# Optimization experiments

Hardware: AMD Instinct MI355X
Metric: run time of the kernel (lower is better)

Reference implementation:

```python
import jax, jax.numpy as jnp
import numpy as np

VOCAB, EMBED, HIDDEN, N_CLASSES = 50257, 128, 256, 2
B = S = 512  # must be equal: the original module only runs when x.size(0)==x.size(1)


def gru_layer(x_seq, Wih, Whh, bih, bhh):
    """PyTorch-equation GRU over time axis 0. x_seq: (T, N, E) -> (T, N, H)."""
    T, N, _ = x_seq.shape
    H = Whh.shape[1]
    xi = x_seq @ Wih.T + bih  # precompute input projections for all steps: (T, N, 3H)

    def step(h, xi_t):
        gh = h @ Whh.T + bhh
        xr, xz, xn = jnp.split(xi_t, 3, axis=-1)
        hr, hz, hn = jnp.split(gh, 3, axis=-1)
        r = jax.nn.sigmoid(xr + hr)
        z = jax.nn.sigmoid(xz + hz)
        n = jnp.tanh(xn + r * hn)
        h_new = (1.0 - z) * n + z * h
        return h_new, h_new

    h0 = jnp.zeros((N, H), dtype=x_seq.dtype)
    _, ys = jax.lax.scan(step, h0, xi)
    return ys


def setup_inputs() -> dict:
    key = jax.random.key(0)
    ks = jax.random.split(key, 12)
    sc = 0.05
    return {
        "x": jax.random.randint(ks[0], (B, S), 0, VOCAB),
        "embed_table": jax.random.normal(ks[1], (VOCAB, EMBED), jnp.float32) * sc,
        "Wih0": jax.random.normal(ks[2], (3 * HIDDEN, EMBED), jnp.float32) * sc,
        "Whh0": jax.random.normal(ks[3], (3 * HIDDEN, HIDDEN), jnp.float32) * sc,
        "bih0": jax.random.normal(ks[4], (3 * HIDDEN,), jnp.float32) * sc,
        "bhh0": jax.random.normal(ks[5], (3 * HIDDEN,), jnp.float32) * sc,
        "Wih1": jax.random.normal(ks[6], (3 * HIDDEN, HIDDEN), jnp.float32) * sc,
        "Whh1": jax.random.normal(ks[7], (3 * HIDDEN, HIDDEN), jnp.float32) * sc,
        "bih1": jax.random.normal(ks[8], (3 * HIDDEN,), jnp.float32) * sc,
        "bhh1": jax.random.normal(ks[9], (3 * HIDDEN,), jnp.float32) * sc,
        "W_out": jax.random.normal(ks[10], (N_CLASSES, HIDDEN), jnp.float32) * sc,
        "b_out": jax.random.normal(ks[11], (N_CLASSES,), jnp.float32) * sc,
    }


def reference(x, embed_table, Wih0, Whh0, bih0, bhh0, Wih1, Whh1, bih1, bhh1, W_out, b_out):
    emb = embed_table[x]                 # (B, S, E)
    # nn.GRU default batch_first=False: dim 0 (=B) is TIME, dim 1 (=S) is batch.
    y = gru_layer(emb, Wih0, Whh0, bih0, bhh0)   # (B, S, H)
    y = gru_layer(y, Wih1, Whh1, bih1, bhh1)     # (B, S, H)
    h_t = y[:, -1, :]                    # (B, H)
    # self.dropout(h_t) in the original discards its result -> no-op.
    logit = h_t @ W_out.T + b_out        # (B, n_classes)
    return logit
```

## Files before the change

kernel.cpp:

```cpp
#include <hip/hip_runtime.h>
#include <hip/hip_fp16.h>

typedef _Float16 f16x2 __attribute__((ext_vector_type(2)));
typedef _Float16 half8 __attribute__((ext_vector_type(8)));

#define TS  512
#define HID 256
#define G3  768
#define EMB 128
#define NB1 8
#define RPB 96
#define CTL 767
#define BSZ 8
#define WAITN 8

__device__ __forceinline__ float sigmoidf_(float x){ return 1.0f/(1.0f+__expf(-x)); }
__device__ __forceinline__ float tanhf_(float x){
  float e = __expf(-2.0f*fabsf(x));
  float t = (1.0f-e)/(1.0f+e);
  return copysignf(t,x);
}

#define SHUF(V,A,B) __builtin_shufflevector(V,V,A,B)
#define WR32(X) X(0,0) X(0,1) X(0,2) X(0,3) X(1,0) X(1,1) X(1,2) X(1,3) \
                X(2,0) X(2,1) X(2,2) X(2,3) X(3,0) X(3,1) X(3,2) X(3,3) \
                X(4,0) X(4,1) X(4,2) X(4,3) X(5,0) X(5,1) X(5,2) X(5,3) \
                X(6,0) X(6,1) X(6,2) X(6,3) X(7,0) X(7,1) X(7,2) X(7,3)

template<int MODE>
__device__ __forceinline__ void rec_layer(const float* __restrict__ Whh,
    const float* __restrict__ bhh, const float* __restrict__ xi,
    _Float16* __restrict__ h16out, float* __restrict__ f32out,
    unsigned* __restrict__ flagB, unsigned* __restrict__ cntWait,
    _Float16 (*hbuf)[8*40], float* gh, float* bhhL)
{
  int tid = threadIdx.x;
  int g   = tid >> 3;
  int o   = tid & 7;

#define WDECL(I,C) half8 w##I##_##C;
  WR32(WDECL)
#define WLOAD(I,C) { \
    const float4* p_ = (const float4*)(Whh + (long)(8*g+(I))*HID + 32*o + 8*(C)); \
    float4 u_ = p_[0], v_ = p_[1]; \
    w##I##_##C = (half8){(_Float16)u_.x,(_Float16)u_.y,(_Float16)u_.z,(_Float16)u_.w, \
                         (_Float16)v_.x,(_Float16)v_.y,(_Float16)v_.z,(_Float16)v_.w}; }
  WR32(WLOAD)

  float hprev = 0.f;
  float xr=0.f, xz=0.f, xn=0.f;
  bhhL[tid] = bhh[tid];
  if (tid < 80) ((half8*)hbuf)[tid] = (half8)(_Float16)0;

  if (tid == CTL){
    while (__hip_atomic_load(&cntWait[0], __ATOMIC_RELAXED, __HIP_MEMORY_SCOPE_AGENT) < WAITN)
      __builtin_amdgcn_s_sleep(1);
    __threadfence();
  }
  __syncthreads();
  if (tid < HID){
    xr = xi[tid]; xz = xi[HID+tid]; xn = xi[2*HID+tid];
  }

  for (int t = 0; t < TS; t++){
    if (tid == CTL && ((t+1) & (BSZ-1)) == 0 && t+1 < TS){
      unsigned b = (unsigned)(t+1) >> 3;
      while (__hip_atomic_load(&cntWait[b], __ATOMIC_RELAXED, __HIP_MEMORY_SCOPE_AGENT) < WAITN)
        __builtin_amdgcn_s_sleep(1);
      __threadfence();
    }

    const half8* hp = (const half8*)(&hbuf[t & 1][o*40]);
    float a0=0.f,a1=0.f,a2=0.f,a3=0.f,a4=0.f,a5=0.f,a6=0.f,a7=0.f;
#define DOT1(I,C,HV) \
    a##I = __builtin_amdgcn_fdot2(SHUF(w##I##_##C,0,1), SHUF(HV,0,1), a##I, false); \
    a##I = __builtin_amdgcn_fdot2(SHUF(w##I##_##C,2,3), SHUF(HV,2,3), a##I, false); \
    a##I = __builtin_amdgcn_fdot2(SHUF(w##I##_##C,4,5), SHUF(HV,4,5), a##I, false); \
    a##I = __builtin_amdgcn_fdot2(SHUF(w##I##_##C,6,7), SHUF(HV,6,7), a##I, false);
#define DOTCHUNK(C) { half8 hv = hp[C]; \
    DOT1(0,C,hv) DOT1(1,C,hv) DOT1(2,C,hv) DOT1(3,C,hv) \
    DOT1(4,C,hv) DOT1(5,C,hv) DOT1(6,C,hv) DOT1(7,C,hv) }
    DOTCHUNK(0) DOTCHUNK(1) DOTCHUNK(2) DOTCHUNK(3)

    bool b0 = o & 1, b1 = o & 2, b2 = o & 4;
    float s, r_;
    s = b0 ? a0 : a1; r_ = __shfl_xor(s, 1, 64); float c0 = (b0 ? a1 : a0) + r_;
    s = b0 ? a2 : a3; r_ = __shfl_xor(s, 1, 64); float c1 = (b0 ? a3 : a2) + r_;
    s = b0 ? a4 : a5; r_ = __shfl_xor(s, 1, 64); float c2 = (b0 ? a5 : a4) + r_;
    s = b0 ? a6 : a7; r_ = __shfl_xor(s, 1, 64); float c3 = (b0 ? a7 : a6) + r_;
    s = b1 ? c0 : c1; r_ = __shfl_xor(s, 2, 64); float d0 = (b1 ? c1 : c0) + r_;
    s = b1 ? c2 : c3; r_ = __shfl_xor(s, 2, 64); float d1 = (b1 ? c3 : c2) + r_;
    s = b2 ? d0 : d1; r_ = __shfl_xor(s, 4, 64); float e  = (b2 ? d1 : d0) + r_;
    gh[tid] = e;
    __syncthreads();

    if (tid < HID){
      float r = sigmoidf_(xr + bhhL[tid] + gh[tid]);
      float z = sigmoidf_(xz + bhhL[HID+tid] + gh[HID+tid]);
      float n = tanhf_(xn + r*(gh[2*HID+tid] + bhhL[2*HID+tid]));
      float hnew = (1.0f - z)*n + z*hprev;
      hprev = hnew;
      if (MODE == 1) f32out[(long)t*HID + tid] = hnew;
      float partner = __shfl_xor(hnew, 1, 64);
      if ((tid & 1) == 0){
        f16x2 p; p.x = (_Float16)hnew; p.y = (_Float16)partner;
        *(f16x2*)(&hbuf[(t+1)&1][(tid>>5)*40 + (tid&31)]) = p;
        if (MODE == 0) *(f16x2*)(h16out + (long)t*HID + tid) = p;
      }
      if (t+1 < TS){
        const float* xp = xi + (long)(t+1)*G3;
        xr = xp[tid]; xz = xp[HID+tid]; xn = xp[2*HID+tid];
      }
    }
    __syncthreads();
    if (MODE == 0 && tid == CTL && ((t+1) & (BSZ-1)) == 0){
      __threadfence();
      __hip_atomic_store(&flagB[t >> 3], 1u, __ATOMIC_RELEASE, __HIP_MEMORY_SCOPE_AGENT);
    }
  }
}

__device__ __forceinline__ void xi1_stage(const float* __restrict__ Wih1,
    const float* __restrict__ bih1, const _Float16* __restrict__ h16,
    float* __restrict__ xi1, unsigned* __restrict__ flagB,
    unsigned* __restrict__ cntB, int slice)
{
  int tid = threadIdx.x;
  int r = tid >> 3, o = tid & 7;
  int row = slice*RPB + r;
  half8 w0,w1,w2,w3;
  {
    const float4* wp = (const float4*)(Wih1 + (long)row*HID + o*32);
    float4 p0=wp[0],p1=wp[1],p2=wp[2],p3=wp[3],p4=wp[4],p5=wp[5],p6=wp[6],p7=wp[7];
    w0 = (half8){(_Float16)p0.x,(_Float16)p0.y,(_Float16)p0.z,(_Float16)p0.w,
                 (_Float16)p1.x,(_Float16)p1.y,(_Float16)p1.z,(_Float16)p1.w};
    w1 = (half8){(_Float16)p2.x,(_Float16)p2.y,(_Float16)p2.z,(_Float16)p2.w,
                 (_Float16)p3.x,(_Float16)p3.y,(_Float16)p3.z,(_Float16)p3.w};
    w2 = (half8){(_Float16)p4.x,(_Float16)p4.y,(_Float16)p4.z,(_Float16)p4.w,
                 (_Float16)p5.x,(_Float16)p5.y,(_Float16)p5.z,(_Float16)p5.w};
    w3 = (half8){(_Float16)p6.x,(_Float16)p6.y,(_Float16)p6.z,(_Float16)p6.w,
                 (_Float16)p7.x,(_Float16)p7.y,(_Float16)p7.z,(_Float16)p7.w};
  }
  float bias = bih1[row];

  for (int b = 0; b < TS/BSZ; b++){
    if (tid == 0){
      while (__hip_atomic_load(&flagB[b], __ATOMIC_RELAXED, __HIP_MEMORY_SCOPE_AGENT) == 0u)
        __builtin_amdgcn_s_sleep(1);
      __threadfence();
    }
    __syncthreads();
    #pragma unroll 4
    for (int u = 0; u < BSZ; u++){
      int t = b*BSZ + u;
      const half8* hp = (const half8*)(h16 + (long)t*HID + o*32);
      half8 h0 = hp[0], h1 = hp[1], h2 = hp[2], h3 = hp[3];
      float acc = 0.f;
#define XDOT(W,H) \
      acc = __builtin_amdgcn_fdot2(SHUF(W,0,1), SHUF(H,0,1), acc, false); \
      acc = __builtin_amdgcn_fdot2(SHUF(W,2,3), SHUF(H,2,3), acc, false); \
      acc = __builtin_amdgcn_fdot2(SHUF(W,4,5), SHUF(H,4,5), acc, false); \
      acc = __builtin_amdgcn_fdot2(SHUF(W,6,7), SHUF(H,6,7), acc, false);
      XDOT(w0,h0) XDOT(w1,h1) XDOT(w2,h2) XDOT(w3,h3)
      acc += __shfl_xor(acc, 1, 64);
      acc += __shfl_xor(acc, 2, 64);
      acc += __shfl_xor(acc, 4, 64);
      if (o == 0) xi1[(long)t*G3 + row] = acc + bias;
    }
    __syncthreads();
    if (tid == 0){
      __threadfence();
      atomicAdd(&cntB[b], 1u);
    }
  }
}

__device__ __forceinline__ void xi0_stage(const int* __restrict__ x,
    const float* __restrict__ emb_tab, const float* __restrict__ Wih0,
    const float* __restrict__ bih0, float* __restrict__ xi0,
    unsigned* __restrict__ cntX, int slice, float* embp)
{
  int tid = threadIdx.x;
  int j = tid >> 3, kk = tid & 7;
  int row = slice*96 + j;
  float w16[16];
  {
    const float4* wp = (const float4*)(Wih0 + (long)row*EMB + kk*16);
    float4 a = wp[0], b = wp[1], c = wp[2], d = wp[3];
    w16[0]=a.x;  w16[1]=a.y;  w16[2]=a.z;  w16[3]=a.w;
    w16[4]=b.x;  w16[5]=b.y;  w16[6]=b.z;  w16[7]=b.w;
    w16[8]=c.x;  w16[9]=c.y;  w16[10]=c.z; w16[11]=c.w;
    w16[12]=d.x; w16[13]=d.y; w16[14]=d.z; w16[15]=d.w;
  }
  float bias = bih0[row];

  for (int t = 0; t < TS; t++){
    if (tid < EMB){
      int idx = x[(long)t*512 + 511];
      embp[tid + (tid >> 4)] = emb_tab[(long)idx*EMB + tid];
    }
    __syncthreads();
    float a = 0.f;
    #pragma unroll
    for (int m = 0; m < 16; m++) a += w16[m] * embp[kk*17 + m];
    a += __shfl_xor(a, 1, 64);
    a += __shfl_xor(a, 2, 64);
    a += __shfl_xor(a, 4, 64);
    if (kk == 0) xi0[(long)t*G3 + row] = a + bias;
    __syncthreads();
    if (((t+1) & (BSZ-1)) == 0 && tid == 0){
      __threadfence();
      atomicAdd(&cntX[t >> 3], 1u);
    }
  }
}

__global__ __launch_bounds__(768, 3)
void pipe_kernel(
    const float* __restrict__ Whh0, const float* __restrict__ bhh0,
    const float* __restrict__ Wih1, const float* __restrict__ bih1,
    const float* __restrict__ Whh1, const float* __restrict__ bhh1,
    const int* __restrict__ x, const float* __restrict__ emb_tab,
    const float* __restrict__ Wih0, const float* __restrict__ bih0,
    float* __restrict__ xi0, _Float16* __restrict__ h1f16,
    float* __restrict__ xi1, float* __restrict__ h2,
    unsigned* __restrict__ flagB, unsigned* __restrict__ cntB,
    unsigned* __restrict__ cntX)
{
  __shared__ __align__(16) _Float16 hbuf[2][8*40];
  __shared__ float gh[G3];
  __shared__ float bhhL[G3];
  __shared__ float embp[136];
  int bid = blockIdx.x;
  if (bid == 0)
    rec_layer<0>(Whh0, bhh0, xi0, h1f16, nullptr, flagB, cntX, hbuf, gh, bhhL);
  else if (bid == 9)
    rec_layer<1>(Whh1, bhh1, xi1, nullptr, h2, flagB, cntB, hbuf, gh, bhhL);
  else if (bid < 9)
    xi1_stage(Wih1, bih1, h1f16, xi1, flagB, cntB, bid - 1);
  else
    xi0_stage(x, emb_tab, Wih0, bih0, xi0, cntX, bid - 10, embp);
}

__global__ __launch_bounds__(1024) void logits_kernel(const float* __restrict__ h2,
    const float* __restrict__ Wout, const float* __restrict__ bout,
    float* __restrict__ out)
{
  __shared__ __align__(16) float wsm[2*HID];
  __shared__ float bs[2];
  int tid = threadIdx.x;
  if (tid < 2*HID) wsm[tid] = Wout[tid];
  if (tid < 2)     bs[tid]  = bout[tid];
  __syncthreads();
  int t = tid >> 1, c = tid & 1;
  const float4* hr = (const float4*)(h2 + (long)t*HID);
  const float4* wr = (const float4*)(wsm + c*HID);
  float acc = bs[c];
  #pragma unroll 8
  for (int m=0;m<HID/4;m++){
    float4 h = hr[m]; float4 wv = wr[m];
    acc += h.x*wv.x + h.y*wv.y + h.z*wv.z + h.w*wv.w;
  }
  out[tid] = acc;
}

extern "C" void kernel_launch(void* const* d_in, const int* in_sizes, int n_in,
                              void* d_out, int out_size, void* d_ws, size_t ws_size,
                              hipStream_t stream)
{
  const int*   x    = (const int*)  d_in[0];
  const float* emb  = (const float*)d_in[1];
  const float* Wih0 = (const float*)d_in[2];
  const float* Whh0 = (const float*)d_in[3];
  const float* bih0 = (const float*)d_in[4];
  const float* bhh0 = (const float*)d_in[5];
  const float* Wih1 = (const float*)d_in[6];
  const float* Whh1 = (const float*)d_in[7];
  const float* bih1 = (const float*)d_in[8];
  const float* bhh1 = (const float*)d_in[9];
  const float* Wout = (const float*)d_in[10];
  const float* bout = (const float*)d_in[11];
  float* out = (float*)d_out;

  char* ws = (char*)d_ws;
  float*     xi0   = (float*)(ws);
  float*     xi1   = (float*)(ws + 1572864);
  _Float16*  h1f16 = (_Float16*)(ws + 3145728);
  float*     h2    = (float*)(ws + 3407872);
  unsigned*  flagB = (unsigned*)(ws + 3932160);
  unsigned*  cntB  = (unsigned*)(ws + 3933184);
  unsigned*  cntX  = (unsigned*)(ws + 3934208);

  hipMemsetAsync(ws + 3932160, 0, 4096, stream);
  pipe_kernel<<<18, 768, 0, stream>>>(Whh0, bhh0, Wih1, bih1, Whh1, bhh1,
                                      x, emb, Wih0, bih0,
                                      xi0, h1f16, xi1, h2, flagB, cntB, cntX);
  logits_kernel<<<1, 1024, 0, stream>>>(h2, Wout, bout, out);
}
```

Measured before the change: 834.9 us.

## Halve pipeline sync block size and fuse logits into layer-2 recurrent block

```diff
diff --git a/kernel.cpp b/kernel.cpp
--- a/kernel.cpp
+++ b/kernel.cpp
@@ -8,10 +8,9 @@
 #define HID 256
 #define G3  768
 #define EMB 128
-#define NB1 8
 #define RPB 96
 #define CTL 767
-#define BSZ 8
+#define BSZ 4
 #define WAITN 8
 
 __device__ __forceinline__ float sigmoidf_(float x){ return 1.0f/(1.0f+__expf(-x)); }
@@ -32,7 +31,9 @@
     const float* __restrict__ bhh, const float* __restrict__ xi,
     _Float16* __restrict__ h16out, float* __restrict__ f32out,
     unsigned* __restrict__ flagB, unsigned* __restrict__ cntWait,
-    _Float16 (*hbuf)[8*40], float* gh, float* bhhL)
+    _Float16 (*hbuf)[8*40], float* gh, float* bhhL,
+    const float* __restrict__ Wout, const float* __restrict__ bout,
+    float* __restrict__ out)
 {
   int tid = threadIdx.x;
   int g   = tid >> 3;
@@ -64,7 +65,7 @@
 
   for (int t = 0; t < TS; t++){
     if (tid == CTL && ((t+1) & (BSZ-1)) == 0 && t+1 < TS){
-      unsigned b = (unsigned)(t+1) >> 3;
+      unsigned b = (unsigned)(t+1) / BSZ;
       while (__hip_atomic_load(&cntWait[b], __ATOMIC_RELAXED, __HIP_MEMORY_SCOPE_AGENT) < WAITN)
         __builtin_amdgcn_s_sleep(1);
       __threadfence();
@@ -115,7 +116,23 @@
     __syncthreads();
     if (MODE == 0 && tid == CTL && ((t+1) & (BSZ-1)) == 0){
       __threadfence();
-      __hip_atomic_store(&flagB[t >> 3], 1u, __ATOMIC_RELEASE, __HIP_MEMORY_SCOPE_AGENT);
+      __hip_atomic_store(&flagB[t / BSZ], 1u, __ATOMIC_RELEASE, __HIP_MEMORY_SCOPE_AGENT);
+    }
+  }
+
+  if (MODE == 1){
+    __syncthreads();
+    for (int i = tid; i < 2*TS; i += 768){
+      int t = i >> 1, c = i & 1;
+      const float4* hr = (const float4*)(f32out + (long)t*HID);
+      const float4* wr = (const float4*)(Wout + c*HID);
+      float acc = bout[c];
+      #pragma unroll 8
+      for (int m = 0; m < HID/4; m++){
+        float4 h = hr[m]; float4 wv = wr[m];
+        acc += h.x*wv.x + h.y*wv.y + h.z*wv.z + h.w*wv.w;
+      }
+      out[i] = acc;
     }
   }
 }
@@ -150,7 +167,7 @@
       __threadfence();
     }
     __syncthreads();
-    #pragma unroll 4
+    #pragma unroll
     for (int u = 0; u < BSZ; u++){
       int t = b*BSZ + u;
       const half8* hp = (const half8*)(h16 + (long)t*HID + o*32);
@@ -210,7 +227,7 @@
     __syncthreads();
     if (((t+1) & (BSZ-1)) == 0 && tid == 0){
       __threadfence();
-      atomicAdd(&cntX[t >> 3], 1u);
+      atomicAdd(&cntX[t / BSZ], 1u);
     }
   }
 }
@@ -222,8 +239,10 @@
     const float* __restrict__ Whh1, const float* __restrict__ bhh1,
     const int* __restrict__ x, const float* __restrict__ emb_tab,
     const float* __restrict__ Wih0, const float* __restrict__ bih0,
+    const float* __restrict__ Wout, const float* __restrict__ bout,
     float* __restrict__ xi0, _Float16* __restrict__ h1f16,
     float* __restrict__ xi1, float* __restrict__ h2,
+    float* __restrict__ out,
     unsigned* __restrict__ flagB, unsigned* __restrict__ cntB,
     unsigned* __restrict__ cntX)
 {
@@ -233,35 +252,15 @@
   __shared__ float embp[136];
   int bid = blockIdx.x;
   if (bid == 0)
-    rec_layer<0>(Whh0, bhh0, xi0, h1f16, nullptr, flagB, cntX, hbuf, gh, bhhL);
+    rec_layer<0>(Whh0, bhh0, xi0, h1f16, nullptr, flagB, cntX, hbuf, gh, bhhL,
+                 nullptr, nullptr, nullptr);
   else if (bid == 9)
-    rec_layer<1>(Whh1, bhh1, xi1, nullptr, h2, flagB, cntB, hbuf, gh, bhhL);
+    rec_layer<1>(Whh1, bhh1, xi1, nullptr, h2, flagB, cntB, hbuf, gh, bhhL,
+                 Wout, bout, out);
   else if (bid < 9)
     xi1_stage(Wih1, bih1, h1f16, xi1, flagB, cntB, bid - 1);
   else
     xi0_stage(x, emb_tab, Wih0, bih0, xi0, cntX, bid - 10, embp);
-}
-
-__global__ __launch_bounds__(1024) void logits_kernel(const float* __restrict__ h2,
-    const float* __restrict__ Wout, const float* __restrict__ bout,
-    float* __restrict__ out)
-{
-  __shared__ __align__(16) float wsm[2*HID];
-  __shared__ float bs[2];
-  int tid = threadIdx.x;
-  if (tid < 2*HID) wsm[tid] = Wout[tid];
-  if (tid < 2)     bs[tid]  = bout[tid];
-  __syncthreads();
-  int t = tid >> 1, c = tid & 1;
-  const float4* hr = (const float4*)(h2 + (long)t*HID);
-  const float4* wr = (const float4*)(wsm + c*HID);
-  float acc = bs[c];
-  #pragma unroll 8
-  for (int m=0;m<HID/4;m++){
-    float4 h = hr[m]; float4 wv = wr[m];
-    acc += h.x*wv.x + h.y*wv.y + h.z*wv.z + h.w*wv.w;
-  }
-  out[tid] = acc;
 }
 
 extern "C" void kernel_launch(void* const* d_in, const int* in_sizes, int n_in,
@@ -293,7 +292,7 @@
 
   hipMemsetAsync(ws + 3932160, 0, 4096, stream);
   pipe_kernel<<<18, 768, 0, stream>>>(Whh0, bhh0, Wih1, bih1, Whh1, bhh1,
-                                      x, emb, Wih0, bih0,
-                                      xi0, h1f16, xi1, h2, flagB, cntB, cntX);
-  logits_kernel<<<1, 1024, 0, stream>>>(h2, Wout, bout, out);
-}
+                                      x, emb, Wih0, bih0, Wout, bout,
+                                      xi0, h1f16, xi1, h2, out,
+                                      flagB, cntB, cntX);
+}
```

Result: no change. 839.5 us (+0.5%).
